# Optimization experiments

Hardware: AMD Instinct MI355X
Metric: run time of the kernel (lower is better)

Reference implementation:

```python
import jax, jax.numpy as jnp
import numpy as np

EMBED_DIM = 128
N_EMBED = 10000
INPUT_SHAPE = (8, 64, 32, EMBED_DIM)


def setup_inputs() -> dict:
    key = jax.random.key(0)
    k1, k2 = jax.random.split(key)
    inputs = jax.random.normal(k1, INPUT_SHAPE, dtype=jnp.float32)
    cluster_mean = jax.random.normal(k2, (EMBED_DIM, N_EMBED), dtype=jnp.float32)
    return {"inputs": inputs, "cluster_mean": cluster_mean}


def reference(inputs, cluster_mean):
    embed_dim = cluster_mean.shape[0]
    # Flatten all leading dims: (N, D)
    samples = inputs.reshape(-1, embed_dim)
    # Squared euclidean distance to each code: (N, n_embed)
    dist = (
        jnp.sum(samples ** 2, axis=1, keepdims=True)
        - 2.0 * samples @ cluster_mean
        + jnp.sum(cluster_mean ** 2, axis=0, keepdims=True)
    )
    cluster_index = jnp.argmin(dist, axis=1).reshape(inputs.shape[:-1])
    # Embedding lookup from transposed codebook: (..., D)
    quantize = cluster_mean.T[cluster_index]
    q_loss = jnp.mean((quantize - jax.lax.stop_gradient(inputs)) ** 2)
    e_loss = jnp.mean((jax.lax.stop_gradient(quantize) - inputs) ** 2)
    loss = q_loss + 0.25 * e_loss
    # Straight-through estimator
    outputs = inputs + jax.lax.stop_gradient(quantize - inputs)
    return outputs, loss
```

## Files before the change

kernel.cpp:

```cpp
#include <hip/hip_runtime.h>

#define EMBED 128
#define NCODE 10000
#define NSAMP 16384
#define NCODE_PAD 10240
#define NSPLIT 8
#define SPLIT_CODES 1280
#define NCHUNK 40
#define CHUNK_ELEMS 4096
#define OUT_ELEMS (NSAMP * EMBED)
#define TAU 0.002f
#define NSEG 16

typedef float f32x16 __attribute__((ext_vector_type(16)));
typedef short s16x8 __attribute__((ext_vector_type(8)));
typedef unsigned short ushort_t;
typedef unsigned long long u64;

#define OFF_AH  0
#define OFF_AL  2621440
#define OFF_CT  5242880
#define OFF_CN  10485760
#define OFF_KEY 10526720
#define OFF_C2  11575296
#define OFF_IDX 12099584
#define OFF_RL  12165120
#define OFF_CNT 12230656
#define OFF_BEST 12230720

__device__ __forceinline__ unsigned short f2bf(float f) {
    unsigned u = __float_as_uint(f);
    return (unsigned short)((u + 0x7fffu + ((u >> 16) & 1u)) >> 16);
}
__device__ __forceinline__ float bf2f(unsigned short h) {
    return __uint_as_float(((unsigned)h) << 16);
}
__device__ __forceinline__ unsigned ordf(float f) {
    unsigned u = __float_as_uint(f);
    return (u & 0x80000000u) ? ~u : (u | 0x80000000u);
}
__device__ __forceinline__ float unordf(unsigned o) {
    return __uint_as_float((o & 0x80000000u) ? (o ^ 0x80000000u) : ~o);
}

__global__ __launch_bounds__(256) void prep_a(const float* __restrict__ C,
                                              ushort_t* __restrict__ Ah,
                                              ushort_t* __restrict__ Al,
                                              float* __restrict__ CT,
                                              float* __restrict__ out,
                                              int* __restrict__ counter) {
    int o = blockIdx.x * 256 + threadIdx.x;
    if (o == 0) { out[OUT_ELEMS] = 0.f; *counter = 0; }
    const int n  = o % NCODE_PAD;
    const int kg = o / NCODE_PAD;
    const int split = n / SPLIT_CODES;
    const int rem   = n % SPLIT_CODES;
    const int chunk = rem >> 5;
    const int row   = rem & 31;
    const size_t eoff = (size_t)(split * NCHUNK + chunk) * CHUNK_ELEMS
                      + (size_t)kg * 256 + row * 8;
    const int k0 = kg * 8;
    float f[8];
    s16x8 vh, vl;
#pragma unroll
    for (int j = 0; j < 8; ++j) {
        float v = (n < NCODE) ? C[(size_t)(k0 + j) * NCODE + n] : 0.f;
        f[j] = v;
        unsigned short h = f2bf(v);
        vh[j] = (short)h;
        vl[j] = (short)f2bf(v - bf2f(h));
    }
    *(float4*)(CT + (size_t)n * EMBED + k0)     = make_float4(f[0], f[1], f[2], f[3]);
    *(float4*)(CT + (size_t)n * EMBED + k0 + 4) = make_float4(f[4], f[5], f[6], f[7]);
    *(s16x8*)(Ah + eoff) = vh;
    *(s16x8*)(Al + eoff) = vl;
}

__global__ __launch_bounds__(256) void prep_n(const float* __restrict__ CT,
                                              float* __restrict__ cnorm) {
    const int t = threadIdx.x;
    const int n = blockIdx.x * 8 + (t >> 5);
    const int l = t & 31;
    float4 v = *(const float4*)(CT + (size_t)n * EMBED + l * 4);
    float s = v.x * v.x + v.y * v.y + v.z * v.z + v.w * v.w;
#pragma unroll
    for (int off = 1; off < 32; off <<= 1) s += __shfl_xor(s, off, 32);
    if (l == 0) cnorm[n] = (n < NCODE) ? s : 3.0e38f;
}

__global__ __launch_bounds__(256)
void vq11(const float* __restrict__ X,
          const ushort_t* __restrict__ Ah,
          const ushort_t* __restrict__ Al,
          const float* __restrict__ cnorm,
          u64* __restrict__ candKey,
          unsigned* __restrict__ cand2) {
    __shared__ ushort_t Bs[2 * 2 * CHUNK_ELEMS];
    const int t    = threadIdx.x;
    const int lane = t & 63;
    const int wave = t >> 6;
    const int ln   = lane & 31;
    const int kh   = lane >> 5;
    const int split = blockIdx.y;
    const int m0    = blockIdx.x * 128;

    s16x8 bh[8], bl[8];
    {
        const int m = m0 + wave * 32 + ln;
#pragma unroll
        for (int ks = 0; ks < 8; ++ks) {
            const float* src = X + (size_t)m * EMBED + ks * 16 + kh * 8;
            float4 f0 = *(const float4*)src;
            float4 f1 = *(const float4*)(src + 4);
            float f[8] = {f0.x, f0.y, f0.z, f0.w, f1.x, f1.y, f1.z, f1.w};
            s16x8 vh, vl;
#pragma unroll
            for (int j = 0; j < 8; ++j) {
                float v = -2.f * f[j];
                unsigned short h = f2bf(v);
                vh[j] = (short)h;
                vl[j] = (short)f2bf(v - bf2f(h));
            }
            bh[ks] = vh;
            bl[ks] = vl;
        }
    }

    float v1 = 3.4e38f, v2 = 3.4e38f;
    int   j1 = 0;

    auto ldsw = (__attribute__((address_space(3))) ushort_t*)Bs;
    const int woff = wave * 1024;
    const size_t chbase = (size_t)(split * NCHUNK) * CHUNK_ELEMS;

    {
        const ushort_t* sh = Ah + chbase + woff + lane * 8;
        const ushort_t* sl = Al + chbase + woff + lane * 8;
#pragma unroll
        for (int i = 0; i < 2; ++i) {
            __builtin_amdgcn_global_load_lds(
                (const __attribute__((address_space(1))) void*)(sh + i * 512),
                (__attribute__((address_space(3))) void*)(ldsw + woff + i * 512),
                16, 0, 0);
            __builtin_amdgcn_global_load_lds(
                (const __attribute__((address_space(1))) void*)(sl + i * 512),
                (__attribute__((address_space(3))) void*)(ldsw + CHUNK_ELEMS + woff + i * 512),
                16, 0, 0);
        }
    }
    __syncthreads();

    for (int c = 0; c < NCHUNK; ++c) {
        const int b = c & 1;
        if (c + 1 < NCHUNK) {
            const size_t sb = chbase + (size_t)(c + 1) * CHUNK_ELEMS;
            const ushort_t* sh = Ah + sb + woff + lane * 8;
            const ushort_t* sl = Al + sb + woff + lane * 8;
            const int db = (1 - b) * 2 * CHUNK_ELEMS + woff;
#pragma unroll
            for (int i = 0; i < 2; ++i) {
                __builtin_amdgcn_global_load_lds(
                    (const __attribute__((address_space(1))) void*)(sh + i * 512),
                    (__attribute__((address_space(3))) void*)(ldsw + db + i * 512),
                    16, 0, 0);
                __builtin_amdgcn_global_load_lds(
                    (const __attribute__((address_space(1))) void*)(sl + i * 512),
                    (__attribute__((address_space(3))) void*)(ldsw + db + CHUNK_ELEMS + i * 512),
                    16, 0, 0);
            }
        }

        const int bb = b * 2 * CHUNK_ELEMS;

        f32x16 accA = {0,0,0,0,0,0,0,0,0,0,0,0,0,0,0,0};
        f32x16 accB = {0,0,0,0,0,0,0,0,0,0,0,0,0,0,0,0};
#pragma unroll
        for (int ks = 0; ks < 4; ++ks) {
            const int foA = bb + (ks * 2 + kh) * 256 + ln * 8;
            const int foB = bb + ((ks + 4) * 2 + kh) * 256 + ln * 8;
            s16x8 aAh = *(const s16x8*)&Bs[foA];
            s16x8 aAl = *(const s16x8*)&Bs[CHUNK_ELEMS + foA];
            s16x8 aBh = *(const s16x8*)&Bs[foB];
            s16x8 aBl = *(const s16x8*)&Bs[CHUNK_ELEMS + foB];
            accA = __builtin_amdgcn_mfma_f32_32x32x16_bf16(aAh, bh[ks], accA, 0, 0, 0);
            accB = __builtin_amdgcn_mfma_f32_32x32x16_bf16(aBh, bh[ks + 4], accB, 0, 0, 0);
            accA = __builtin_amdgcn_mfma_f32_32x32x16_bf16(aAh, bl[ks], accA, 0, 0, 0);
            accB = __builtin_amdgcn_mfma_f32_32x32x16_bf16(aBh, bl[ks + 4], accB, 0, 0, 0);
            accA = __builtin_amdgcn_mfma_f32_32x32x16_bf16(aAl, bh[ks], accA, 0, 0, 0);
            accB = __builtin_amdgcn_mfma_f32_32x32x16_bf16(aBl, bh[ks + 4], accB, 0, 0, 0);
        }
        const int cbase = split * SPLIT_CODES + c * 32 + 4 * kh;
#pragma unroll
        for (int r = 0; r < 16; ++r) {
            const int code = cbase + ((r & 3) + 8 * (r >> 2));
            const float cn = cnorm[code];
            float d = (accA[r] + accB[r]) + cn;
            if (d < v1) { v2 = v1; v1 = d; j1 = code; }
            else        { v2 = fminf(v2, d); }
        }
        __syncthreads();
    }

    {
        float ov1 = __shfl_xor(v1, 32, 64);
        int   oj1 = __shfl_xor(j1, 32, 64);
        float ov2 = __shfl_xor(v2, 32, 64);
        float hi = fmaxf(v1, ov1);
        v2 = fminf(fminf(v2, ov2), hi);
        if (ov1 < v1 || (ov1 == v1 && oj1 < j1)) { v1 = ov1; j1 = oj1; }
        if (kh == 0) {
            int m = m0 + wave * 32 + ln;
            candKey[(size_t)m * NSPLIT + split] =
                ((u64)ordf(v1) << 32) | (unsigned)j1;
            cand2[(size_t)m * NSPLIT + split] = ordf(v2);
        }
    }
}

__global__ __launch_bounds__(256) void outfin_k(const float* __restrict__ X,
                                                const float* __restrict__ CT,
                                                const u64* __restrict__ candKey,
                                                const unsigned* __restrict__ cand2,
                                                int* __restrict__ idxf,
                                                int* __restrict__ rlist,
                                                int* __restrict__ counter,
                                                u64* __restrict__ wsBest,
                                                float* __restrict__ out) {
    __shared__ float red[4];
    const int t = threadIdx.x;
    const int m = blockIdx.x * 8 + (t >> 5);
    const int l = t & 31;

    int code = 0;
    if (l == 0) {
        u64 best = 0xffffffffffffffffull;
        float v2 = 3.4e38f;
#pragma unroll
        for (int s = 0; s < NSPLIT; ++s) {
            u64 k = candKey[(size_t)m * NSPLIT + s];
            unsigned o2 = cand2[(size_t)m * NSPLIT + s];
            if (k < best) {
                if (best != 0xffffffffffffffffull)
                    v2 = fminf(v2, unordf((unsigned)(best >> 32)));
                best = k;
                v2 = fminf(v2, unordf(o2));
            } else {
                v2 = fminf(v2, unordf((unsigned)(k >> 32)));
            }
        }
        code = (int)(unsigned)(best & 0xffffffffu);
        idxf[m] = code;
        float v1 = unordf((unsigned)(best >> 32));
        if (v2 - v1 <= TAU) {
            rlist[atomicAdd(counter, 1)] = m;
            wsBest[m] = 0xffffffffffffffffull;
        }
    }
    code = __shfl(code, 0, 32);

    float4 q = *(const float4*)(CT + (size_t)code * EMBED + l * 4);
    float4 x = *(const float4*)(X + (size_t)m * EMBED + l * 4);
    *(float4*)(out + (size_t)m * EMBED + l * 4) = q;
    float dx = q.x - x.x, dy = q.y - x.y, dz = q.z - x.z, dw = q.w - x.w;
    float lsum = dx * dx + dy * dy + dz * dz + dw * dw;
#pragma unroll
    for (int off = 1; off < 64; off <<= 1) lsum += __shfl_xor(lsum, off, 64);
    if ((t & 63) == 0) red[t >> 6] = lsum;
    __syncthreads();
    if (t == 0)
        atomicAdd(out + OUT_ELEMS,
                  (red[0] + red[1] + red[2] + red[3]) * (1.25f / (float)OUT_ELEMS));
}

__global__ __launch_bounds__(256) void rescue_seg(const float* __restrict__ X,
                                                  const float* __restrict__ CT,
                                                  const float* __restrict__ cnorm,
                                                  const int* __restrict__ rlist,
                                                  const int* __restrict__ counter,
                                                  u64* __restrict__ wsBest) {
    __shared__ float xs[EMBED];
    __shared__ u64 wk[4];
    const int t = threadIdx.x;
    const int lane = t & 63;
    const int wave = t >> 6;
    const int hw = t & 31;
    const int slot = t >> 5;
    const int cnt = *counter;
    const int nw = cnt * NSEG;

    for (int w = blockIdx.x; w < nw; w += gridDim.x) {
        const int s = w >> 4, seg = w & 15;
        const int m = rlist[s];
        __syncthreads();
        if (t < 32) {
            float4 v = *(const float4*)(X + (size_t)m * EMBED + t * 4);
            xs[t * 4 + 0] = v.x; xs[t * 4 + 1] = v.y;
            xs[t * 4 + 2] = v.z; xs[t * 4 + 3] = v.w;
        }
        __syncthreads();
        const float x0 = xs[hw * 4 + 0], x1 = xs[hw * 4 + 1];
        const float x2 = xs[hw * 4 + 2], x3 = xs[hw * 4 + 3];
        const int base = seg * 625;
        const int jend = base + 625;
        u64 bk = 0xffffffffffffffffull;
        for (int it = 0; it < 20; ++it) {
            const int r0 = base + it * 32 + slot * 4;
            float4 c0, c1, c2, c3;
            bool ok0 = (r0 + 0 < jend), ok1 = (r0 + 1 < jend);
            bool ok2 = (r0 + 2 < jend), ok3 = (r0 + 3 < jend);
            c0 = ok0 ? *(const float4*)(CT + (size_t)(r0 + 0) * EMBED + hw * 4) : make_float4(0, 0, 0, 0);
            c1 = ok1 ? *(const float4*)(CT + (size_t)(r0 + 1) * EMBED + hw * 4) : make_float4(0, 0, 0, 0);
            c2 = ok2 ? *(const float4*)(CT + (size_t)(r0 + 2) * EMBED + hw * 4) : make_float4(0, 0, 0, 0);
            c3 = ok3 ? *(const float4*)(CT + (size_t)(r0 + 3) * EMBED + hw * 4) : make_float4(0, 0, 0, 0);
            float p0 = x0 * c0.x, p1 = x0 * c1.x, p2 = x0 * c2.x, p3 = x0 * c3.x;
            p0 = fmaf(x1, c0.y, p0); p1 = fmaf(x1, c1.y, p1);
            p2 = fmaf(x1, c2.y, p2); p3 = fmaf(x1, c3.y, p3);
            p0 = fmaf(x2, c0.z, p0); p1 = fmaf(x2, c1.z, p1);
            p2 = fmaf(x2, c2.z, p2); p3 = fmaf(x2, c3.z, p3);
            p0 = fmaf(x3, c0.w, p0); p1 = fmaf(x3, c1.w, p1);
            p2 = fmaf(x3, c2.w, p2); p3 = fmaf(x3, c3.w, p3);
#pragma unroll
            for (int off = 1; off < 32; off <<= 1) {
                p0 += __shfl_xor(p0, off, 32);
                p1 += __shfl_xor(p1, off, 32);
                p2 += __shfl_xor(p2, off, 32);
                p3 += __shfl_xor(p3, off, 32);
            }
            if (hw == 0) {
                if (ok0) { u64 k = ((u64)ordf(fmaf(-2.f, p0, cnorm[r0 + 0])) << 32) | (unsigned)(r0 + 0); if (k < bk) bk = k; }
                if (ok1) { u64 k = ((u64)ordf(fmaf(-2.f, p1, cnorm[r0 + 1])) << 32) | (unsigned)(r0 + 1); if (k < bk) bk = k; }
                if (ok2) { u64 k = ((u64)ordf(fmaf(-2.f, p2, cnorm[r0 + 2])) << 32) | (unsigned)(r0 + 2); if (k < bk) bk = k; }
                if (ok3) { u64 k = ((u64)ordf(fmaf(-2.f, p3, cnorm[r0 + 3])) << 32) | (unsigned)(r0 + 3); if (k < bk) bk = k; }
            }
        }
#pragma unroll
        for (int off = 1; off < 64; off <<= 1) {
            u64 o = __shfl_xor(bk, off, 64);
            if (o < bk) bk = o;
        }
        if (lane == 0) wk[wave] = bk;
        __syncthreads();
        if (t == 0) {
            u64 b = wk[0];
            if (wk[1] < b) b = wk[1];
            if (wk[2] < b) b = wk[2];
            if (wk[3] < b) b = wk[3];
            atomicMin(&wsBest[m], b);
        }
    }
}

__global__ __launch_bounds__(256) void patch_k(const float* __restrict__ X,
                                               const float* __restrict__ CT,
                                               const int* __restrict__ rlist,
                                               const int* __restrict__ counter,
                                               const u64* __restrict__ wsBest,
                                               const int* __restrict__ idxf,
                                               float* __restrict__ out) {
    const int t = threadIdx.x;
    const int l = t & 31, sl = t >> 5;
    const int cnt = *counter;
    for (int s = blockIdx.x * 8 + sl; s < cnt; s += gridDim.x * 8) {
        int m = rlist[s];
        u64 key = wsBest[m];
        int jn = (int)(unsigned)(key & 0xffffffffu);
        int jo = idxf[m];
        if (jn == jo) continue;
        float4 qn = *(const float4*)(CT + (size_t)jn * EMBED + l * 4);
        float4 qo = *(const float4*)(CT + (size_t)jo * EMBED + l * 4);
        float4 x  = *(const float4*)(X + (size_t)m * EMBED + l * 4);
        *(float4*)(out + (size_t)m * EMBED + l * 4) = qn;
        float dn = (qn.x - x.x) * (qn.x - x.x) + (qn.y - x.y) * (qn.y - x.y)
                 + (qn.z - x.z) * (qn.z - x.z) + (qn.w - x.w) * (qn.w - x.w);
        float dp = (qo.x - x.x) * (qo.x - x.x) + (qo.y - x.y) * (qo.y - x.y)
                 + (qo.z - x.z) * (qo.z - x.z) + (qo.w - x.w) * (qo.w - x.w);
        float delta = dn - dp;
#pragma unroll
        for (int off = 1; off < 32; off <<= 1) delta += __shfl_xor(delta, off, 32);
        if (l == 0)
            atomicAdd(out + OUT_ELEMS, delta * (1.25f / (float)OUT_ELEMS));
    }
}

extern "C" void kernel_launch(void* const* d_in, const int* in_sizes, int n_in,
                              void* d_out, int out_size, void* d_ws, size_t ws_size,
                              hipStream_t stream) {
    const float* X = (const float*)d_in[0];
    const float* C = (const float*)d_in[1];
    float* out = (float*)d_out;
    char* ws = (char*)d_ws;

    ushort_t* Ah = (ushort_t*)(ws + OFF_AH);
    ushort_t* Al = (ushort_t*)(ws + OFF_AL);
    float* CT    = (float*)(ws + OFF_CT);
    float* cnorm = (float*)(ws + OFF_CN);
    u64* candKey = (u64*)(ws + OFF_KEY);
    unsigned* cand2 = (unsigned*)(ws + OFF_C2);
    int* idxf    = (int*)(ws + OFF_IDX);
    int* rlist   = (int*)(ws + OFF_RL);
    int* counter = (int*)(ws + OFF_CNT);
    u64* wsBest  = (u64*)(ws + OFF_BEST);

    prep_a<<<(NCODE_PAD * 16) / 256, 256, 0, stream>>>(C, Ah, Al, CT, out, counter);
    prep_n<<<NCODE_PAD / 8, 256, 0, stream>>>(CT, cnorm);
    vq11<<<dim3(NSAMP / 128, NSPLIT), 256, 0, stream>>>(X, Ah, Al, cnorm, candKey, cand2);
    outfin_k<<<NSAMP / 8, 256, 0, stream>>>(X, CT, candKey, cand2, idxf, rlist, counter, wsBest, out);
    rescue_seg<<<1024, 256, 0, stream>>>(X, CT, cnorm, rlist, counter, wsBest);
    patch_k<<<64, 256, 0, stream>>>(X, CT, rlist, counter, wsBest, idxf, out);
}
```

Measured before the change: 269.2 us.

## Defer argmin epilogue by one chunk and merge rescue with patch kernel

The main VQ kernel now uses one accumulator chain per chunk and runs the argmin/top-2 epilogue for the previous chunk's results while the current chunk's MFMAs execute, so MFMA latency overlaps with the scalar compare work. The ambiguous-sample rescue pass changes from 16 segments per sample with an atomicMin to one block per sample scanning the whole codebook, and the patch step is folded into that same kernel. This removes one launch and the wsBest buffer, but each rescue block does serial work across all codes and the MFMA chain is now longer and dependent.

```diff
diff --git a/kernel.cpp b/kernel.cpp
--- a/kernel.cpp
+++ b/kernel.cpp
@@ -10,7 +10,6 @@
 #define CHUNK_ELEMS 4096
 #define OUT_ELEMS (NSAMP * EMBED)
 #define TAU 0.002f
-#define NSEG 16
 
 typedef float f32x16 __attribute__((ext_vector_type(16)));
 typedef short s16x8 __attribute__((ext_vector_type(8)));
@@ -26,7 +25,6 @@
 #define OFF_IDX 12099584
 #define OFF_RL  12165120
 #define OFF_CNT 12230656
-#define OFF_BEST 12230720
 
 __device__ __forceinline__ unsigned short f2bf(float f) {
     unsigned u = __float_as_uint(f);
@@ -89,7 +87,7 @@
 }
 
 __global__ __launch_bounds__(256)
-void vq11(const float* __restrict__ X,
+void vq12(const float* __restrict__ X,
           const ushort_t* __restrict__ Ah,
           const ushort_t* __restrict__ Al,
           const float* __restrict__ cnorm,
@@ -150,6 +148,10 @@
     }
     __syncthreads();
 
+    f32x16 accP;
+#pragma unroll
+    for (int r = 0; r < 16; ++r) accP[r] = 3.4e38f;
+
     for (int c = 0; c < NCHUNK; ++c) {
         const int b = c & 1;
         if (c + 1 < NCHUNK) {
@@ -172,33 +174,42 @@
 
         const int bb = b * 2 * CHUNK_ELEMS;
 
-        f32x16 accA = {0,0,0,0,0,0,0,0,0,0,0,0,0,0,0,0};
-        f32x16 accB = {0,0,0,0,0,0,0,0,0,0,0,0,0,0,0,0};
-#pragma unroll
-        for (int ks = 0; ks < 4; ++ks) {
-            const int foA = bb + (ks * 2 + kh) * 256 + ln * 8;
-            const int foB = bb + ((ks + 4) * 2 + kh) * 256 + ln * 8;
-            s16x8 aAh = *(const s16x8*)&Bs[foA];
-            s16x8 aAl = *(const s16x8*)&Bs[CHUNK_ELEMS + foA];
-            s16x8 aBh = *(const s16x8*)&Bs[foB];
-            s16x8 aBl = *(const s16x8*)&Bs[CHUNK_ELEMS + foB];
-            accA = __builtin_amdgcn_mfma_f32_32x32x16_bf16(aAh, bh[ks], accA, 0, 0, 0);
-            accB = __builtin_amdgcn_mfma_f32_32x32x16_bf16(aBh, bh[ks + 4], accB, 0, 0, 0);
-            accA = __builtin_amdgcn_mfma_f32_32x32x16_bf16(aAh, bl[ks], accA, 0, 0, 0);
-            accB = __builtin_amdgcn_mfma_f32_32x32x16_bf16(aBh, bl[ks + 4], accB, 0, 0, 0);
-            accA = __builtin_amdgcn_mfma_f32_32x32x16_bf16(aAl, bh[ks], accA, 0, 0, 0);
-            accB = __builtin_amdgcn_mfma_f32_32x32x16_bf16(aBl, bh[ks + 4], accB, 0, 0, 0);
-        }
-        const int cbase = split * SPLIT_CODES + c * 32 + 4 * kh;
+        f32x16 acc = {0,0,0,0,0,0,0,0,0,0,0,0,0,0,0,0};
+#pragma unroll
+        for (int ks = 0; ks < 8; ++ks) {
+            const int fo = bb + (ks * 2 + kh) * 256 + ln * 8;
+            s16x8 a_h = *(const s16x8*)&Bs[fo];
+            s16x8 a_l = *(const s16x8*)&Bs[CHUNK_ELEMS + fo];
+            acc = __builtin_amdgcn_mfma_f32_32x32x16_bf16(a_h, bh[ks], acc, 0, 0, 0);
+            acc = __builtin_amdgcn_mfma_f32_32x32x16_bf16(a_h, bl[ks], acc, 0, 0, 0);
+            acc = __builtin_amdgcn_mfma_f32_32x32x16_bf16(a_l, bh[ks], acc, 0, 0, 0);
+        }
+
+        if (c > 0) {
+            const int cbaseP = split * SPLIT_CODES + (c - 1) * 32 + 4 * kh;
+#pragma unroll
+            for (int r = 0; r < 16; ++r) {
+                const int code = cbaseP + ((r & 3) + 8 * (r >> 2));
+                const float cn = cnorm[code];
+                float d = accP[r] + cn;
+                if (d < v1) { v2 = v1; v1 = d; j1 = code; }
+                else        { v2 = fminf(v2, d); }
+            }
+        }
+        accP = acc;
+        __syncthreads();
+    }
+
+    {
+        const int cbaseP = split * SPLIT_CODES + (NCHUNK - 1) * 32 + 4 * kh;
 #pragma unroll
         for (int r = 0; r < 16; ++r) {
-            const int code = cbase + ((r & 3) + 8 * (r >> 2));
+            const int code = cbaseP + ((r & 3) + 8 * (r >> 2));
             const float cn = cnorm[code];
-            float d = (accA[r] + accB[r]) + cn;
+            float d = accP[r] + cn;
             if (d < v1) { v2 = v1; v1 = d; j1 = code; }
             else        { v2 = fminf(v2, d); }
         }
-        __syncthreads();
     }
 
     {
@@ -224,7 +235,6 @@
                                                 int* __restrict__ idxf,
                                                 int* __restrict__ rlist,
                                                 int* __restrict__ counter,
-                                                u64* __restrict__ wsBest,
                                                 float* __restrict__ out) {
     __shared__ float red[4];
     const int t = threadIdx.x;
@@ -251,10 +261,7 @@
         code = (int)(unsigned)(best & 0xffffffffu);
         idxf[m] = code;
         float v1 = unordf((unsigned)(best >> 32));
-        if (v2 - v1 <= TAU) {
-            rlist[atomicAdd(counter, 1)] = m;
-            wsBest[m] = 0xffffffffffffffffull;
-        }
+        if (v2 - v1 <= TAU) rlist[atomicAdd(counter, 1)] = m;
     }
     code = __shfl(code, 0, 32);
 
@@ -272,24 +279,24 @@
                   (red[0] + red[1] + red[2] + red[3]) * (1.25f / (float)OUT_ELEMS));
 }
 
-__global__ __launch_bounds__(256) void rescue_seg(const float* __restrict__ X,
-                                                  const float* __restrict__ CT,
-                                                  const float* __restrict__ cnorm,
-                                                  const int* __restrict__ rlist,
-                                                  const int* __restrict__ counter,
-                                                  u64* __restrict__ wsBest) {
+__global__ __launch_bounds__(256) void rescue_full(const float* __restrict__ X,
+                                                   const float* __restrict__ CT,
+                                                   const float* __restrict__ cnorm,
+                                                   const int* __restrict__ rlist,
+                                                   const int* __restrict__ counter,
+                                                   const int* __restrict__ idxf,
+                                                   float* __restrict__ out) {
     __shared__ float xs[EMBED];
     __shared__ u64 wk[4];
+    __shared__ int sjn;
     const int t = threadIdx.x;
     const int lane = t & 63;
     const int wave = t >> 6;
     const int hw = t & 31;
     const int slot = t >> 5;
     const int cnt = *counter;
-    const int nw = cnt * NSEG;
-
-    for (int w = blockIdx.x; w < nw; w += gridDim.x) {
-        const int s = w >> 4, seg = w & 15;
+
+    for (int s = blockIdx.x; s < cnt; s += gridDim.x) {
         const int m = rlist[s];
         __syncthreads();
         if (t < 32) {
@@ -300,14 +307,12 @@
         __syncthreads();
         const float x0 = xs[hw * 4 + 0], x1 = xs[hw * 4 + 1];
         const float x2 = xs[hw * 4 + 2], x3 = xs[hw * 4 + 3];
-        const int base = seg * 625;
-        const int jend = base + 625;
         u64 bk = 0xffffffffffffffffull;
-        for (int it = 0; it < 20; ++it) {
-            const int r0 = base + it * 32 + slot * 4;
+        for (int it = 0; it < 313; ++it) {
+            const int r0 = it * 32 + slot * 4;
             float4 c0, c1, c2, c3;
-            bool ok0 = (r0 + 0 < jend), ok1 = (r0 + 1 < jend);
-            bool ok2 = (r0 + 2 < jend), ok3 = (r0 + 3 < jend);
+            bool ok0 = (r0 + 0 < NCODE), ok1 = (r0 + 1 < NCODE);
+            bool ok2 = (r0 + 2 < NCODE), ok3 = (r0 + 3 < NCODE);
             c0 = ok0 ? *(const float4*)(CT + (size_t)(r0 + 0) * EMBED + hw * 4) : make_float4(0, 0, 0, 0);
             c1 = ok1 ? *(const float4*)(CT + (size_t)(r0 + 1) * EMBED + hw * 4) : make_float4(0, 0, 0, 0);
             c2 = ok2 ? *(const float4*)(CT + (size_t)(r0 + 2) * EMBED + hw * 4) : make_float4(0, 0, 0, 0);
@@ -345,40 +350,27 @@
             if (wk[1] < b) b = wk[1];
             if (wk[2] < b) b = wk[2];
             if (wk[3] < b) b = wk[3];
-            atomicMin(&wsBest[m], b);
-        }
-    }
-}
-
-__global__ __launch_bounds__(256) void patch_k(const float* __restrict__ X,
-                                               const float* __restrict__ CT,
-                                               const int* __restrict__ rlist,
-                                               const int* __restrict__ counter,
-                                               const u64* __restrict__ wsBest,
-                                               const int* __restrict__ idxf,
-                                               float* __restrict__ out) {
-    const int t = threadIdx.x;
-    const int l = t & 31, sl = t >> 5;
-    const int cnt = *counter;
-    for (int s = blockIdx.x * 8 + sl; s < cnt; s += gridDim.x * 8) {
-        int m = rlist[s];
-        u64 key = wsBest[m];
-        int jn = (int)(unsigned)(key & 0xffffffffu);
-        int jo = idxf[m];
-        if (jn == jo) continue;
-        float4 qn = *(const float4*)(CT + (size_t)jn * EMBED + l * 4);
-        float4 qo = *(const float4*)(CT + (size_t)jo * EMBED + l * 4);
-        float4 x  = *(const float4*)(X + (size_t)m * EMBED + l * 4);
-        *(float4*)(out + (size_t)m * EMBED + l * 4) = qn;
-        float dn = (qn.x - x.x) * (qn.x - x.x) + (qn.y - x.y) * (qn.y - x.y)
-                 + (qn.z - x.z) * (qn.z - x.z) + (qn.w - x.w) * (qn.w - x.w);
-        float dp = (qo.x - x.x) * (qo.x - x.x) + (qo.y - x.y) * (qo.y - x.y)
-                 + (qo.z - x.z) * (qo.z - x.z) + (qo.w - x.w) * (qo.w - x.w);
-        float delta = dn - dp;
-#pragma unroll
-        for (int off = 1; off < 32; off <<= 1) delta += __shfl_xor(delta, off, 32);
-        if (l == 0)
-            atomicAdd(out + OUT_ELEMS, delta * (1.25f / (float)OUT_ELEMS));
+            sjn = (int)(unsigned)(b & 0xffffffffu);
+        }
+        __syncthreads();
+        const int jn = sjn;
+        const int jo = idxf[m];
+        if (jn != jo && t < 32) {
+            float4 qn = *(const float4*)(CT + (size_t)jn * EMBED + t * 4);
+            float4 qo = *(const float4*)(CT + (size_t)jo * EMBED + t * 4);
+            float xa = xs[t * 4 + 0], xb = xs[t * 4 + 1];
+            float xc = xs[t * 4 + 2], xd = xs[t * 4 + 3];
+            *(float4*)(out + (size_t)m * EMBED + t * 4) = qn;
+            float dn = (qn.x - xa) * (qn.x - xa) + (qn.y - xb) * (qn.y - xb)
+                     + (qn.z - xc) * (qn.z - xc) + (qn.w - xd) * (qn.w - xd);
+            float dp = (qo.x - xa) * (qo.x - xa) + (qo.y - xb) * (qo.y - xb)
+                     + (qo.z - xc) * (qo.z - xc) + (qo.w - xd) * (qo.w - xd);
+            float delta = dn - dp;
+#pragma unroll
+            for (int off = 1; off < 32; off <<= 1) delta += __shfl_xor(delta, off, 32);
+            if (t == 0)
+                atomicAdd(out + OUT_ELEMS, delta * (1.25f / (float)OUT_ELEMS));
+        }
     }
 }
 
@@ -399,12 +391,10 @@
     int* idxf    = (int*)(ws + OFF_IDX);
     int* rlist   = (int*)(ws + OFF_RL);
     int* counter = (int*)(ws + OFF_CNT);
-    u64* wsBest  = (u64*)(ws + OFF_BEST);
 
     prep_a<<<(NCODE_PAD * 16) / 256, 256, 0, stream>>>(C, Ah, Al, CT, out, counter);
     prep_n<<<NCODE_PAD / 8, 256, 0, stream>>>(CT, cnorm);
-    vq11<<<dim3(NSAMP / 128, NSPLIT), 256, 0, stream>>>(X, Ah, Al, cnorm, candKey, cand2);
-    outfin_k<<<NSAMP / 8, 256, 0, stream>>>(X, CT, candKey, cand2, idxf, rlist, counter, wsBest, out);
-    rescue_seg<<<1024, 256, 0, stream>>>(X, CT, cnorm, rlist, counter, wsBest);
-    patch_k<<<64, 256, 0, stream>>>(X, CT, rlist, counter, wsBest, idxf, out);
-}
+    vq12<<<dim3(NSAMP / 128, NSPLIT), 256, 0, stream>>>(X, Ah, Al, cnorm, candKey, cand2);
+    outfin_k<<<NSAMP / 8, 256, 0, stream>>>(X, CT, candKey, cand2, idxf, rlist, counter, out);
+    rescue_full<<<1024, 256, 0, stream>>>(X, CT, cnorm, rlist, counter, idxf, out);
+}
```

After: 622.2 us. 2.31x slower.
